# Kernel tuning notes

Measured on AMD Instinct MI355X. Metric: run time of the kernel, lower is better.

The kernel has to match this reference:

```python
import jax, jax.numpy as jnp
import numpy as np

D_MODEL = 1024
N_HEADS = 16
HEAD_DIM = D_MODEL // N_HEADS


def setup_inputs() -> dict:
    key = jax.random.key(0)
    ks = jax.random.split(key, 5)
    x = jax.random.normal(ks[0], (4, 2048, D_MODEL), dtype=jnp.float32)
    s = 1.0 / np.sqrt(D_MODEL)
    W_qkv = jax.random.normal(ks[1], (D_MODEL, 3 * D_MODEL), dtype=jnp.float32) * s
    b_qkv = jnp.zeros((3 * D_MODEL,), dtype=jnp.float32)
    W_proj = jax.random.normal(ks[2], (D_MODEL, D_MODEL), dtype=jnp.float32) * s
    b_proj = jnp.zeros((D_MODEL,), dtype=jnp.float32)
    return {"x": x, "W_qkv": W_qkv, "b_qkv": b_qkv, "W_proj": W_proj, "b_proj": b_proj}


def reference(x, W_qkv, b_qkv, W_proj, b_proj):
    B, T, C = x.shape
    H, Dh = N_HEADS, HEAD_DIM
    qkv = x @ W_qkv + b_qkv                      # [B,T,3C]
    q, k, v = jnp.split(qkv, 3, axis=-1)
    # [B,T,C] -> [B,H,T,Dh]
    q = q.reshape(B, T, H, Dh).transpose(0, 2, 1, 3)
    k = k.reshape(B, T, H, Dh).transpose(0, 2, 1, 3)
    v = v.reshape(B, T, H, Dh).transpose(0, 2, 1, 3)
    scale = 1.0 / np.sqrt(Dh)
    att = jnp.einsum("bhqd,bhkd->bhqk", q, k) * scale
    causal = jnp.tril(jnp.ones((T, T), dtype=bool))
    att = jnp.where(causal, att, -jnp.inf)
    att = jax.nn.softmax(att, axis=-1)
    y = jnp.einsum("bhqk,bhkd->bhqd", att, v)    # [B,H,T,Dh]
    y = y.transpose(0, 2, 1, 3).reshape(B, T, C)
    return y @ W_proj + b_proj
```

## Files before the change

### kernel.cpp

```cpp
#include <hip/hip_runtime.h>
#include <hip/hip_bf16.h>
#include <cstdint>
#include <math.h>

#define DM   1024
#define NH   16
#define DH   64
#define BB   4
#define TT   2048
#define MTOT (BB*TT)

using short8 = __attribute__((ext_vector_type(8))) short;
using f32x4  = __attribute__((ext_vector_type(4))) float;

__device__ __forceinline__ f32x4 mfma16(short8 a, short8 b, f32x4 c) {
  return __builtin_amdgcn_mfma_f32_16x16x32_bf16(a, b, c, 0, 0, 0);
}

typedef const __attribute__((address_space(1))) unsigned int* as1_u32p;
typedef __attribute__((address_space(3))) unsigned int*       as3_u32p;

__device__ __forceinline__ void gl_lds16(const void* g, void* l) {
  __builtin_amdgcn_global_load_lds(
      (as1_u32p)(reinterpret_cast<uintptr_t>(g)),
      (as3_u32p)((unsigned int)(reinterpret_cast<uintptr_t>(l))),
      16, 0, 0);
}

__device__ __forceinline__ int swz64(int row, int col) {
  return row*64 + ((((col >> 3) ^ (row & 7)) << 3) | (col & 7));
}

__device__ __forceinline__ unsigned pkbf(float a, float b) {
  __hip_bfloat162 h = __float22bfloat162_rn(make_float2(a, b));
  return *reinterpret_cast<unsigned*>(&h);
}

__device__ __forceinline__ short8 ldsr_o0(unsigned a) {
  short8 r; asm volatile("ds_read_b128 %0, %1" : "=v"(r) : "v"(a)); return r;
}
__device__ __forceinline__ short8 ldsr_o1(unsigned a) {
  short8 r; asm volatile("ds_read_b128 %0, %1 offset:2048" : "=v"(r) : "v"(a)); return r;
}
__device__ __forceinline__ short8 ldsr_o2(unsigned a) {
  short8 r; asm volatile("ds_read_b128 %0, %1 offset:4096" : "=v"(r) : "v"(a)); return r;
}
__device__ __forceinline__ short8 ldsr_o3(unsigned a) {
  short8 r; asm volatile("ds_read_b128 %0, %1 offset:6144" : "=v"(r) : "v"(a)); return r;
}

#define LGKM0  do { asm volatile("s_waitcnt lgkmcnt(0)"); __builtin_amdgcn_sched_barrier(0); } while(0)
#define VMCNT6 do { __builtin_amdgcn_sched_barrier(0); asm volatile("s_waitcnt vmcnt(6)"); __builtin_amdgcn_sched_barrier(0); } while(0)
#define VMCNT0 do { __builtin_amdgcn_sched_barrier(0); asm volatile("s_waitcnt vmcnt(0)"); __builtin_amdgcn_sched_barrier(0); } while(0)
#define BARRIER do { __builtin_amdgcn_s_barrier(); __builtin_amdgcn_sched_barrier(0); } while(0)

__global__ __launch_bounds__(256) void k_cvt(const float* __restrict__ in,
                                             __hip_bfloat16* __restrict__ out, int n8) {
  int i = blockIdx.x * 256 + threadIdx.x;
  if (i >= n8) return;
  const float* p = in + (size_t)i * 8;
  short8 o;
#pragma unroll
  for (int j = 0; j < 8; ++j) {
    __hip_bfloat16 h = __float2bfloat16(p[j]);
    o[j] = *reinterpret_cast<short*>(&h);
  }
  *reinterpret_cast<short8*>(out + (size_t)i * 8) = o;
}

__global__ __launch_bounds__(256) void k_transpose_cvt(const float* __restrict__ W,
                                                       __hip_bfloat16* __restrict__ Wt,
                                                       int K, int N) {
  __shared__ float tbuf[32][33];
  const int n0 = blockIdx.x * 32, k0 = blockIdx.y * 32;
  const int tx = threadIdx.x & 31, ty = threadIdx.x >> 5;
#pragma unroll
  for (int i = 0; i < 4; ++i)
    tbuf[ty + i*8][tx] = W[(size_t)(k0 + ty + i*8) * N + n0 + tx];
  __syncthreads();
#pragma unroll
  for (int i = 0; i < 4; ++i)
    Wt[(size_t)(n0 + ty + i*8) * K + k0 + tx] = __float2bfloat16(tbuf[tx][ty + i*8]);
}

__global__ __launch_bounds__(512, 2) void k_gemm2(const __hip_bfloat16* __restrict__ A,
                                                  const __hip_bfloat16* __restrict__ Bt,
                                                  const float* __restrict__ bias,
                                                  __hip_bfloat16* __restrict__ Qb,
                                                  __hip_bfloat16* __restrict__ Kb,
                                                  __hip_bfloat16* __restrict__ Vtb) {
  __shared__ __hip_bfloat16 As[3][256 * 64];
  __shared__ __hip_bfloat16 Bs[3][128 * 64];
  const int tid = threadIdx.x;
  const int l = tid & 63, w = tid >> 6;
  const int lr = l & 15, lg = l >> 4;
  const int wm = w >> 1, wn = w & 1;
  const int m0 = blockIdx.x * 256, n0 = blockIdx.y * 128;

  const int srow = tid >> 3;
  const int scol = (((tid & 7) ^ (srow & 7)) << 3);
  const size_t aoffs = (size_t)(m0 + srow) * 1024 + scol;
  const size_t boffs = (size_t)(n0 + srow) * 1024 + scol;
  const int ldst = tid * 8;

  auto stage = [&](int t, int s) {
    const int k0 = t * 64;
    __hip_bfloat16* as_ = &As[s][0];
    __hip_bfloat16* bs_ = &Bs[s][0];
#pragma unroll
    for (int rd = 0; rd < 4; ++rd)
      gl_lds16(A + aoffs + (size_t)rd * 65536 + k0, as_ + rd * 4096 + ldst);
#pragma unroll
    for (int rd = 0; rd < 2; ++rd)
      gl_lds16(Bt + boffs + (size_t)rd * 65536 + k0, bs_ + rd * 4096 + ldst);
  };

  const unsigned asLds = (unsigned)(uintptr_t)&As[0][0];
  const unsigned bsLds = (unsigned)(uintptr_t)&Bs[0][0];
  const unsigned aBase = asLds + 2u * ((wm*64 + lr) * 64 + ((lg ^ (lr & 7)) << 3));
  const unsigned bBase = bsLds + 2u * ((wn*64 + lr) * 64 + ((lg ^ (lr & 7)) << 3));

  stage(0, 0);
  stage(1, 1);
  VMCNT6;
  BARRIER;

  f32x4 acc[4][4] = {};
  short8 a_[4][2], b_[2][2];

#pragma unroll
  for (int t = 0; t < 16; ++t) {
    const int s = t % 3;
    const unsigned aB0 = aBase + (unsigned)s * 32768u;
    const unsigned aB1 = aB0 ^ 64u;
    const unsigned bB0 = bBase + (unsigned)s * 16384u;
    const unsigned bB1 = bB0 ^ 64u;
    if (t + 2 < 16) stage(t + 2, (t + 2) % 3);
    a_[0][0] = ldsr_o0(aB0); a_[1][0] = ldsr_o1(aB0); a_[2][0] = ldsr_o2(aB0); a_[3][0] = ldsr_o3(aB0);
    a_[0][1] = ldsr_o0(aB1); a_[1][1] = ldsr_o1(aB1); a_[2][1] = ldsr_o2(aB1); a_[3][1] = ldsr_o3(aB1);
    b_[0][0] = ldsr_o0(bB0); b_[1][0] = ldsr_o1(bB0);
    b_[0][1] = ldsr_o0(bB1); b_[1][1] = ldsr_o1(bB1);
    LGKM0;
    __builtin_amdgcn_s_setprio(1);
#pragma unroll
    for (int m = 0; m < 4; ++m)
#pragma unroll
      for (int n = 0; n < 2; ++n)
#pragma unroll
        for (int ks = 0; ks < 2; ++ks)
          acc[m][n] = mfma16(a_[m][ks], b_[n][ks], acc[m][n]);
    __builtin_amdgcn_s_setprio(0);
    b_[0][0] = ldsr_o2(bB0); b_[1][0] = ldsr_o3(bB0);
    b_[0][1] = ldsr_o2(bB1); b_[1][1] = ldsr_o3(bB1);
    LGKM0;
    __builtin_amdgcn_s_setprio(1);
#pragma unroll
    for (int m = 0; m < 4; ++m)
#pragma unroll
      for (int n = 0; n < 2; ++n)
#pragma unroll
        for (int ks = 0; ks < 2; ++ks)
          acc[m][n + 2] = mfma16(a_[m][ks], b_[n][ks], acc[m][n + 2]);
    __builtin_amdgcn_s_setprio(0);
    if (t <= 13) { VMCNT6; }
    else if (t == 14) { VMCNT0; }
    BARRIER;
  }

  __syncthreads();
  __hip_bfloat16* reg = &As[0][0] + w * 4096;
  const int colbase = n0 + wn * 64;
  const int which = colbase >> 10;
  const int hh = (colbase >> 6) & 15;
  const float qs = 0.18033688011112042f;
#pragma unroll
  for (int n = 0; n < 4; ++n) {
    const int lc = n * 16 + lr;
    const float bv = bias[colbase + lc];
#pragma unroll
    for (int m = 0; m < 4; ++m) {
#pragma unroll
      for (int r = 0; r < 4; ++r) {
        const int lrow = m * 16 + lg * 4 + r;
        float v = acc[m][n][r] + bv;
        if (which == 0) v *= qs;
        const __hip_bfloat16 hv = __float2bfloat16(v);
        if (which == 2) reg[swz64(lc, lrow)] = hv;
        else            reg[swz64(lrow, lc)] = hv;
      }
    }
  }
  const int rowbase = m0 + wm * 64;
  const int b = rowbase >> 11;
  const size_t bh = (size_t)b * 16 + hh;
  const int g = l >> 2, i = l & 3;
  if (which < 2) {
    __hip_bfloat16* base = (which == 0) ? Qb : Kb;
#pragma unroll
    for (int j = 0; j < 4; ++j) {
      const int lrow = j * 16 + g;
      const int t = (rowbase & 2047) + lrow;
      __hip_bfloat16* dst = base + (bh * TT + t) * 64 + i * 16;
      short8 y0 = *reinterpret_cast<const short8*>(&reg[swz64(lrow, i * 16)]);
      short8 y1 = *reinterpret_cast<const short8*>(&reg[swz64(lrow, i * 16 + 8)]);
      *reinterpret_cast<short8*>(dst) = y0;
      *reinterpret_cast<short8*>(dst + 8) = y1;
    }
  } else {
#pragma unroll
    for (int j = 0; j < 4; ++j) {
      const int dd = j * 16 + g;
      const int t = (rowbase & 2047) + i * 16;
      __hip_bfloat16* dst = Vtb + (bh * 64 + dd) * TT + t;
      short8 y0 = *reinterpret_cast<const short8*>(&reg[swz64(dd, i * 16)]);
      short8 y1 = *reinterpret_cast<const short8*>(&reg[swz64(dd, i * 16 + 8)]);
      *reinterpret_cast<short8*>(dst) = y0;
      *reinterpret_cast<short8*>(dst + 8) = y1;
    }
  }
}

__global__ __launch_bounds__(256) void k_gemm(const __hip_bfloat16* __restrict__ A,
                                              const __hip_bfloat16* __restrict__ Bt,
                                              const float* __restrict__ bias,
                                              float* __restrict__ outF) {
  __shared__ __hip_bfloat16 As[128 * 64];
  __shared__ __hip_bfloat16 Bs[128 * 64];
  const int tid = threadIdx.x;
  const int l = tid & 63, w = tid >> 6;
  const int lr = l & 15, lg = l >> 4;
  const int wr = w >> 1, wc = w & 1;
  const int m0 = blockIdx.x * 128, n0 = blockIdx.y * 128;
  f32x4 acc[4][4] = {};
  for (int k0 = 0; k0 < 1024; k0 += 64) {
#pragma unroll
    for (int it = 0; it < 4; ++it) {
      int e = it * 2048 + tid * 8;
      int row = e >> 6;
      int lcol = ((((e >> 3) & 7) ^ (row & 7)) << 3);
      gl_lds16(A + (size_t)(m0 + row) * 1024 + k0 + lcol, &As[e]);
    }
#pragma unroll
    for (int it = 0; it < 4; ++it) {
      int e = it * 2048 + tid * 8;
      int row = e >> 6;
      int lcol = ((((e >> 3) & 7) ^ (row & 7)) << 3);
      gl_lds16(Bt + (size_t)(n0 + row) * 1024 + k0 + lcol, &Bs[e]);
    }
    __syncthreads();
#pragma unroll
    for (int ks = 0; ks < 2; ++ks) {
      short8 af[4], bf[4];
#pragma unroll
      for (int m = 0; m < 4; ++m)
        af[m] = *reinterpret_cast<const short8*>(&As[swz64(wr*64 + m*16 + lr, ks*32 + lg*8)]);
#pragma unroll
      for (int n = 0; n < 4; ++n)
        bf[n] = *reinterpret_cast<const short8*>(&Bs[swz64(wc*64 + n*16 + lr, ks*32 + lg*8)]);
#pragma unroll
      for (int m = 0; m < 4; ++m)
#pragma unroll
        for (int n = 0; n < 4; ++n)
          acc[m][n] = mfma16(af[m], bf[n], acc[m][n]);
    }
    __syncthreads();
  }
#pragma unroll
  for (int n = 0; n < 4; ++n) {
    const int col = n0 + wc*64 + n*16 + lr;
    const float bv = bias[col];
#pragma unroll
    for (int m = 0; m < 4; ++m)
#pragma unroll
      for (int r = 0; r < 4; ++r) {
        const int row = m0 + wr*64 + m*16 + lg*4 + r;
        outF[(size_t)row * 1024 + col] = acc[m][n][r] + bv;
      }
  }
}

__device__ __forceinline__ void attn_chunks(const __hip_bfloat16* __restrict__ Klds,
                                            const __hip_bfloat16* __restrict__ Vtlds,
                                            int ka, int va0, int va1, int va2, int va3,
                                            int kv0, int kmaxw, int qm,
                                            short8 qf0, short8 qf1,
                                            f32x4 (&acc)[4], float& lrun) {
  const int vak[4] = {va0, va1, va2, va3};
#pragma unroll
  for (int kci = 0; kci < 4; ++kci) {
    const int kbase = kv0 + kci * 32;
    if (kbase > kmaxw) break;
    f32x4 s0 = {}, s1 = {};
    {
      const int kb = ka + kci * 2048;
      short8 kf00 = *reinterpret_cast<const short8*>(&Klds[kb]);
      short8 kf10 = *reinterpret_cast<const short8*>(&Klds[kb + 1024]);
      short8 kf01 = *reinterpret_cast<const short8*>(&Klds[kb ^ 32]);
      short8 kf11 = *reinterpret_cast<const short8*>(&Klds[(kb + 1024) ^ 32]);
      s0 = mfma16(kf00, qf0, s0);
      s1 = mfma16(kf10, qf0, s1);
      s0 = mfma16(kf01, qf1, s0);
      s1 = mfma16(kf11, qf1, s1);
    }
    if (kbase + 31 > kmaxw - 15) {
#pragma unroll
      for (int r = 0; r < 4; ++r) {
        if (kbase + r > qm)      s0[r] = -INFINITY;
        if (kbase + 16 + r > qm) s1[r] = -INFINITY;
      }
    }
    float p0 = __builtin_amdgcn_exp2f(s0[0]), p1 = __builtin_amdgcn_exp2f(s0[1]);
    float p2 = __builtin_amdgcn_exp2f(s0[2]), p3 = __builtin_amdgcn_exp2f(s0[3]);
    float p4 = __builtin_amdgcn_exp2f(s1[0]), p5 = __builtin_amdgcn_exp2f(s1[1]);
    float p6 = __builtin_amdgcn_exp2f(s1[2]), p7 = __builtin_amdgcn_exp2f(s1[3]);
    lrun += ((p0 + p1) + (p2 + p3)) + ((p4 + p5) + (p6 + p7));
    unsigned u0 = pkbf(p0, p1);
    unsigned u1 = pkbf(p2, p3);
    unsigned u2 = pkbf(p4, p5);
    unsigned u3 = pkbf(p6, p7);
    const int l = threadIdx.x & 63;
    const int lr = l & 15, lg = l >> 4;
    const int sa = (((lg & 1) << 1) << 4) + lr;
    const int sb = sa + 16;
    unsigned va_0 = (unsigned)__shfl((int)u0, sa), va_1 = (unsigned)__shfl((int)u1, sa);
    unsigned va_2 = (unsigned)__shfl((int)u2, sa), va_3 = (unsigned)__shfl((int)u3, sa);
    unsigned vb_0 = (unsigned)__shfl((int)u0, sb), vb_1 = (unsigned)__shfl((int)u1, sb);
    unsigned vb_2 = (unsigned)__shfl((int)u2, sb), vb_3 = (unsigned)__shfl((int)u3, sb);
    const bool hi = lg >= 2;
    union { unsigned u[4]; short8 s; } pw;
    pw.u[0] = hi ? va_2 : va_0;
    pw.u[1] = hi ? va_3 : va_1;
    pw.u[2] = hi ? vb_2 : vb_0;
    pw.u[3] = hi ? vb_3 : vb_1;
    const short8 pf = pw.s;
    const int vb = vak[kci];
    short8 v0 = *reinterpret_cast<const short8*>(&Vtlds[vb]);
    short8 v1 = *reinterpret_cast<const short8*>(&Vtlds[vb + 2048]);
    short8 v2 = *reinterpret_cast<const short8*>(&Vtlds[vb + 4096]);
    short8 v3 = *reinterpret_cast<const short8*>(&Vtlds[vb + 6144]);
    acc[0] = mfma16(v0, pf, acc[0]);
    acc[1] = mfma16(v1, pf, acc[1]);
    acc[2] = mfma16(v2, pf, acc[2]);
    acc[3] = mfma16(v3, pf, acc[3]);
  }
}

__device__ __forceinline__ void store_tile(__hip_bfloat16* Ylds, f32x4 (&acc)[4],
                                           float lrun, int q0, int w, int l,
                                           int lr, int lg, int bh,
                                           __hip_bfloat16* __restrict__ Y) {
  lrun += __shfl_xor(lrun, 16);
  lrun += __shfl_xor(lrun, 32);
  const float inv = 1.f / lrun;
#pragma unroll
  for (int nb = 0; nb < 4; ++nb) {
#pragma unroll
    for (int r = 0; r < 4; ++r) {
      const int d = nb * 16 + lg * 4 + r;
      Ylds[swz64(lr, d)] = __float2bfloat16(acc[nb][r] * inv);
    }
  }
  const int rr = l >> 2, part = l & 3;
  const int trow = q0 + w * 16 + rr;
  const int b = bh >> 4, h = bh & 15;
  short8 y0 = *reinterpret_cast<const short8*>(&Ylds[swz64(rr, part * 16)]);
  short8 y1 = *reinterpret_cast<const short8*>(&Ylds[swz64(rr, part * 16 + 8)]);
  __hip_bfloat16* dst = Y + ((size_t)b * TT + trow) * 1024 + h * 64 + part * 16;
  *reinterpret_cast<short8*>(dst) = y0;
  *reinterpret_cast<short8*>(dst + 8) = y1;
}

__global__ __launch_bounds__(256, 4) void k_flash(const __hip_bfloat16* __restrict__ Qb,
                                                  const __hip_bfloat16* __restrict__ Kb,
                                                  const __hip_bfloat16* __restrict__ Vtb,
                                                  __hip_bfloat16* __restrict__ Y) {
  __shared__ __hip_bfloat16 Klds[128 * 64];
  __shared__ __hip_bfloat16 Vtlds[64 * 128];
  const int tid = threadIdx.x;
  const int l = tid & 63, w = tid >> 6;
  const int lr = l & 15, lg = l >> 4;
  const int p  = blockIdx.x >> 6;
  const int bh = blockIdx.x & 63;
  const int q0A = p * 64, q0B = (31 - p) * 64;
  const __hip_bfloat16* Qp = Qb + (size_t)bh * TT * 64;
  const __hip_bfloat16* Kp = Kb + (size_t)bh * TT * 64;
  const __hip_bfloat16* Vp = Vtb + (size_t)bh * 64 * TT;
  const int qrowA = q0A + w * 16 + lr;
  const int qrowB = q0B + w * 16 + lr;
  const short8 qfA0 = *reinterpret_cast<const short8*>(Qp + (size_t)qrowA * 64 + lg * 8);
  const short8 qfA1 = *reinterpret_cast<const short8*>(Qp + (size_t)qrowA * 64 + 32 + lg * 8);
  const short8 qfB0 = *reinterpret_cast<const short8*>(Qp + (size_t)qrowB * 64 + lg * 8);
  const short8 qfB1 = *reinterpret_cast<const short8*>(Qp + (size_t)qrowB * 64 + 32 + lg * 8);
  f32x4 accA[4] = {}, accB[4] = {};
  float lA = 0.f, lB = 0.f;

  const int ka  = lr * 64 + ((lg ^ (lr & 7)) << 3);
  const int va  = lr * 128 + ((lg ^ (lr & 15)) << 3);
  const int va1 = va ^ 32, va2 = va ^ 64, va3 = va ^ 96;

  const __hip_bfloat16* gk[4];
  const __hip_bfloat16* gv[4];
  __hip_bfloat16* lk[4];
  __hip_bfloat16* lv[4];
#pragma unroll
  for (int it = 0; it < 4; ++it) {
    int e = it * 2048 + tid * 8;
    int rowk = e >> 6;
    int lcolk = ((((e >> 3) & 7) ^ (rowk & 7)) << 3);
    gk[it] = Kp + (size_t)rowk * 64 + lcolk;
    lk[it] = &Klds[e];
    int rowv = e >> 7;
    int lcolv = ((((e >> 3) & 15) ^ (rowv & 15)) << 3);
    gv[it] = Vp + (size_t)rowv * TT + lcolv;
    lv[it] = &Vtlds[e];
  }

  const int kmaxwA = q0A + w * 16 + 15;
  const int kmaxwB = q0B + w * 16 + 15;
  const int qmA = qrowA - lg * 4;
  const int qmB = qrowB - lg * 4;
  const int nblk = (q0B + 63) / 128 + 1;
  for (int blk = 0; blk < nblk; ++blk) {
    const int kv0 = blk * 128;
#pragma unroll
    for (int it = 0; it < 4; ++it) {
      gl_lds16(gk[it], lk[it]);
      gk[it] += 128 * 64;
    }
#pragma unroll
    for (int it = 0; it < 4; ++it) {
      gl_lds16(gv[it], lv[it]);
      gv[it] += 128;
    }
    __syncthreads();
    if (kv0 <= q0A + 63)
      attn_chunks(Klds, Vtlds, ka, va, va1, va2, va3, kv0, kmaxwA, qmA, qfA0, qfA1, accA, lA);
    attn_chunks(Klds, Vtlds, ka, va, va1, va2, va3, kv0, kmaxwB, qmB, qfB0, qfB1, accB, lB);
    __syncthreads();
  }
  __hip_bfloat16* Ylds = Klds + w * 1024;
  store_tile(Ylds, accA, lA, q0A, w, l, lr, lg, bh, Y);
  store_tile(Ylds, accB, lB, q0B, w, l, lr, lg, bh, Y);
}

extern "C" void kernel_launch(void* const* d_in, const int* in_sizes, int n_in,
                              void* d_out, int out_size, void* d_ws, size_t ws_size,
                              hipStream_t stream) {
  const float* x     = (const float*)d_in[0];
  const float* Wqkv  = (const float*)d_in[1];
  const float* bqkv  = (const float*)d_in[2];
  const float* Wproj = (const float*)d_in[3];
  const float* bproj = (const float*)d_in[4];

  char* ws = (char*)d_ws;
  size_t off = 0;
  auto alloc = [&](size_t bytes) {
    char* p = ws + off;
    off += (bytes + 255) & ~(size_t)255;
    return p;
  };
  __hip_bfloat16* xb    = (__hip_bfloat16*)alloc((size_t)MTOT * 1024 * 2);
  __hip_bfloat16* wqkvT = (__hip_bfloat16*)alloc((size_t)3072 * 1024 * 2);
  __hip_bfloat16* wpT   = (__hip_bfloat16*)alloc((size_t)1024 * 1024 * 2);
  __hip_bfloat16* Qb    = (__hip_bfloat16*)alloc((size_t)64 * TT * 64 * 2);
  __hip_bfloat16* Kb    = (__hip_bfloat16*)alloc((size_t)64 * TT * 64 * 2);
  __hip_bfloat16* Vtb   = (__hip_bfloat16*)alloc((size_t)64 * TT * 64 * 2);
  __hip_bfloat16* Yb    = (__hip_bfloat16*)alloc((size_t)MTOT * 1024 * 2);

  k_cvt<<<(MTOT * 1024 / 8 + 255) / 256, 256, 0, stream>>>(x, xb, MTOT * 1024 / 8);
  k_transpose_cvt<<<dim3(3072 / 32, 1024 / 32), 256, 0, stream>>>(Wqkv, wqkvT, 1024, 3072);
  k_transpose_cvt<<<dim3(1024 / 32, 1024 / 32), 256, 0, stream>>>(Wproj, wpT, 1024, 1024);
  k_gemm2<<<dim3(32, 24), 512, 0, stream>>>(xb, wqkvT, bqkv, Qb, Kb, Vtb);
  k_flash<<<16 * 64, 256, 0, stream>>>(Qb, Kb, Vtb, Yb);
  k_gemm<<<dim3(64, 8), 256, 0, stream>>>(Yb, wpT, bproj, (float*)d_out);
}
```

Baseline: 168.0 us.

## Share K/V fragment loads across both query tiles and use permlane swaps

```diff
diff --git a/kernel.cpp b/kernel.cpp
--- a/kernel.cpp
+++ b/kernel.cpp
@@ -34,6 +34,16 @@
 __device__ __forceinline__ unsigned pkbf(float a, float b) {
   __hip_bfloat162 h = __float22bfloat162_rn(make_float2(a, b));
   return *reinterpret_cast<unsigned*>(&h);
+}
+
+__device__ __forceinline__ unsigned xor16v(unsigned x, bool odd) {
+  unsigned a = x, b = x;
+  asm("v_permlane16_swap_b32 %0, %1" : "+v"(a), "+v"(b));
+  return odd ? a : b;
+}
+__device__ __forceinline__ unsigned swap32sel(unsigned d, unsigned s, bool odd) {
+  asm("v_permlane32_swap_b32 %0, %1" : "+v"(d), "+v"(s));
+  return odd ? s : d;
 }
 
 __device__ __forceinline__ short8 ldsr_o0(unsigned a) {
@@ -279,70 +289,47 @@
   }
 }
 
-__device__ __forceinline__ void attn_chunks(const __hip_bfloat16* __restrict__ Klds,
-                                            const __hip_bfloat16* __restrict__ Vtlds,
-                                            int ka, int va0, int va1, int va2, int va3,
-                                            int kv0, int kmaxw, int qm,
-                                            short8 qf0, short8 qf1,
-                                            f32x4 (&acc)[4], float& lrun) {
-  const int vak[4] = {va0, va1, va2, va3};
-#pragma unroll
-  for (int kci = 0; kci < 4; ++kci) {
-    const int kbase = kv0 + kci * 32;
-    if (kbase > kmaxw) break;
-    f32x4 s0 = {}, s1 = {};
-    {
-      const int kb = ka + kci * 2048;
-      short8 kf00 = *reinterpret_cast<const short8*>(&Klds[kb]);
-      short8 kf10 = *reinterpret_cast<const short8*>(&Klds[kb + 1024]);
-      short8 kf01 = *reinterpret_cast<const short8*>(&Klds[kb ^ 32]);
-      short8 kf11 = *reinterpret_cast<const short8*>(&Klds[(kb + 1024) ^ 32]);
-      s0 = mfma16(kf00, qf0, s0);
-      s1 = mfma16(kf10, qf0, s1);
-      s0 = mfma16(kf01, qf1, s0);
-      s1 = mfma16(kf11, qf1, s1);
-    }
-    if (kbase + 31 > kmaxw - 15) {
-#pragma unroll
-      for (int r = 0; r < 4; ++r) {
-        if (kbase + r > qm)      s0[r] = -INFINITY;
-        if (kbase + 16 + r > qm) s1[r] = -INFINITY;
-      }
-    }
-    float p0 = __builtin_amdgcn_exp2f(s0[0]), p1 = __builtin_amdgcn_exp2f(s0[1]);
-    float p2 = __builtin_amdgcn_exp2f(s0[2]), p3 = __builtin_amdgcn_exp2f(s0[3]);
-    float p4 = __builtin_amdgcn_exp2f(s1[0]), p5 = __builtin_amdgcn_exp2f(s1[1]);
-    float p6 = __builtin_amdgcn_exp2f(s1[2]), p7 = __builtin_amdgcn_exp2f(s1[3]);
-    lrun += ((p0 + p1) + (p2 + p3)) + ((p4 + p5) + (p6 + p7));
-    unsigned u0 = pkbf(p0, p1);
-    unsigned u1 = pkbf(p2, p3);
-    unsigned u2 = pkbf(p4, p5);
-    unsigned u3 = pkbf(p6, p7);
-    const int l = threadIdx.x & 63;
-    const int lr = l & 15, lg = l >> 4;
-    const int sa = (((lg & 1) << 1) << 4) + lr;
-    const int sb = sa + 16;
-    unsigned va_0 = (unsigned)__shfl((int)u0, sa), va_1 = (unsigned)__shfl((int)u1, sa);
-    unsigned va_2 = (unsigned)__shfl((int)u2, sa), va_3 = (unsigned)__shfl((int)u3, sa);
-    unsigned vb_0 = (unsigned)__shfl((int)u0, sb), vb_1 = (unsigned)__shfl((int)u1, sb);
-    unsigned vb_2 = (unsigned)__shfl((int)u2, sb), vb_3 = (unsigned)__shfl((int)u3, sb);
-    const bool hi = lg >= 2;
-    union { unsigned u[4]; short8 s; } pw;
-    pw.u[0] = hi ? va_2 : va_0;
-    pw.u[1] = hi ? va_3 : va_1;
-    pw.u[2] = hi ? vb_2 : vb_0;
-    pw.u[3] = hi ? vb_3 : vb_1;
-    const short8 pf = pw.s;
-    const int vb = vak[kci];
-    short8 v0 = *reinterpret_cast<const short8*>(&Vtlds[vb]);
-    short8 v1 = *reinterpret_cast<const short8*>(&Vtlds[vb + 2048]);
-    short8 v2 = *reinterpret_cast<const short8*>(&Vtlds[vb + 4096]);
-    short8 v3 = *reinterpret_cast<const short8*>(&Vtlds[vb + 6144]);
-    acc[0] = mfma16(v0, pf, acc[0]);
-    acc[1] = mfma16(v1, pf, acc[1]);
-    acc[2] = mfma16(v2, pf, acc[2]);
-    acc[3] = mfma16(v3, pf, acc[3]);
-  }
+__device__ __forceinline__ void tile_step(f32x4 s0, f32x4 s1, int kbase, int kmaxw, int qm,
+                                          bool odd, short8 v0, short8 v1, short8 v2, short8 v3,
+                                          f32x4 (&acc)[4], float& lrun) {
+  if (kbase + 31 > kmaxw - 15) {
+#pragma unroll
+    for (int r = 0; r < 4; ++r) {
+      if (kbase + r > qm)      s0[r] = -INFINITY;
+      if (kbase + 16 + r > qm) s1[r] = -INFINITY;
+    }
+  }
+  float p0 = __builtin_amdgcn_exp2f(s0[0]), p1 = __builtin_amdgcn_exp2f(s0[1]);
+  float p2 = __builtin_amdgcn_exp2f(s0[2]), p3 = __builtin_amdgcn_exp2f(s0[3]);
+  float p4 = __builtin_amdgcn_exp2f(s1[0]), p5 = __builtin_amdgcn_exp2f(s1[1]);
+  float p6 = __builtin_amdgcn_exp2f(s1[2]), p7 = __builtin_amdgcn_exp2f(s1[3]);
+  lrun += ((p0 + p1) + (p2 + p3)) + ((p4 + p5) + (p6 + p7));
+  const unsigned u0 = pkbf(p0, p1);
+  const unsigned u1 = pkbf(p2, p3);
+  const unsigned u2 = pkbf(p4, p5);
+  const unsigned u3 = pkbf(p6, p7);
+  const unsigned e0 = xor16v(u0, odd);
+  const unsigned e1 = xor16v(u1, odd);
+  const unsigned e2 = xor16v(u2, odd);
+  const unsigned e3 = xor16v(u3, odd);
+  const unsigned ql0 = odd ? e0 : u0;
+  const unsigned ql1 = odd ? e1 : u1;
+  const unsigned ql2 = odd ? u0 : e0;
+  const unsigned ql3 = odd ? u1 : e1;
+  const unsigned qh0 = odd ? e2 : u2;
+  const unsigned qh1 = odd ? e3 : u3;
+  const unsigned qh2 = odd ? u2 : e2;
+  const unsigned qh3 = odd ? u3 : e3;
+  union { unsigned u[4]; short8 s; } pw;
+  pw.u[0] = swap32sel(ql0, qh0, odd);
+  pw.u[1] = swap32sel(ql1, qh1, odd);
+  pw.u[2] = swap32sel(ql2, qh2, odd);
+  pw.u[3] = swap32sel(ql3, qh3, odd);
+  const short8 pf = pw.s;
+  acc[0] = mfma16(v0, pf, acc[0]);
+  acc[1] = mfma16(v1, pf, acc[1]);
+  acc[2] = mfma16(v2, pf, acc[2]);
+  acc[3] = mfma16(v3, pf, acc[3]);
 }
 
 __device__ __forceinline__ void store_tile(__hip_bfloat16* Ylds, f32x4 (&acc)[4],
@@ -379,6 +366,7 @@
   const int tid = threadIdx.x;
   const int l = tid & 63, w = tid >> 6;
   const int lr = l & 15, lg = l >> 4;
+  const bool odd = (lg & 1);
   const int p  = blockIdx.x >> 6;
   const int bh = blockIdx.x & 63;
   const int q0A = p * 64, q0B = (31 - p) * 64;
@@ -396,7 +384,6 @@
 
   const int ka  = lr * 64 + ((lg ^ (lr & 7)) << 3);
   const int va  = lr * 128 + ((lg ^ (lr & 15)) << 3);
-  const int va1 = va ^ 32, va2 = va ^ 64, va3 = va ^ 96;
 
   const __hip_bfloat16* gk[4];
   const __hip_bfloat16* gv[4];
@@ -433,9 +420,37 @@
       gv[it] += 128;
     }
     __syncthreads();
-    if (kv0 <= q0A + 63)
-      attn_chunks(Klds, Vtlds, ka, va, va1, va2, va3, kv0, kmaxwA, qmA, qfA0, qfA1, accA, lA);
-    attn_chunks(Klds, Vtlds, ka, va, va1, va2, va3, kv0, kmaxwB, qmB, qfB0, qfB1, accB, lB);
+#pragma unroll
+    for (int kci = 0; kci < 4; ++kci) {
+      const int kbase = kv0 + kci * 32;
+      if (kbase > kmaxwB) break;
+      const int kb = ka + kci * 2048;
+      const short8 kf00 = *reinterpret_cast<const short8*>(&Klds[kb]);
+      const short8 kf10 = *reinterpret_cast<const short8*>(&Klds[kb + 1024]);
+      const short8 kf01 = *reinterpret_cast<const short8*>(&Klds[kb ^ 32]);
+      const short8 kf11 = *reinterpret_cast<const short8*>(&Klds[(kb + 1024) ^ 32]);
+      f32x4 sB0 = {}, sB1 = {};
+      sB0 = mfma16(kf00, qfB0, sB0);
+      sB1 = mfma16(kf10, qfB0, sB1);
+      sB0 = mfma16(kf01, qfB1, sB0);
+      sB1 = mfma16(kf11, qfB1, sB1);
+      const bool aAct = (kbase <= kmaxwA);
+      f32x4 sA0 = {}, sA1 = {};
+      if (aAct) {
+        sA0 = mfma16(kf00, qfA0, sA0);
+        sA1 = mfma16(kf10, qfA0, sA1);
+        sA0 = mfma16(kf01, qfA1, sA0);
+        sA1 = mfma16(kf11, qfA1, sA1);
+      }
+      const int vb = va ^ (kci * 32);
+      const short8 v0 = *reinterpret_cast<const short8*>(&Vtlds[vb]);
+      const short8 v1 = *reinterpret_cast<const short8*>(&Vtlds[vb + 2048]);
+      const short8 v2 = *reinterpret_cast<const short8*>(&Vtlds[vb + 4096]);
+      const short8 v3 = *reinterpret_cast<const short8*>(&Vtlds[vb + 6144]);
+      tile_step(sB0, sB1, kbase, kmaxwB, qmB, odd, v0, v1, v2, v3, accB, lB);
+      if (aAct)
+        tile_step(sA0, sA1, kbase, kmaxwA, qmA, odd, v0, v1, v2, v3, accA, lA);
+    }
     __syncthreads();
   }
   __hip_bfloat16* Ylds = Klds + w * 1024;
```

New measurement: 166.3 us. No clear change (-1.0%).
